# Performance work log

Measured on AMD Instinct MI355X. Metric: run time of the kernel, lower is better.

The kernel has to match this reference:

```python
import jax, jax.numpy as jnp
import numpy as np

N_NODES = 100000


def setup_inputs() -> dict:
    key = jax.random.key(0)
    ks = jax.random.split(key, 7)
    input_dim, hidden_dim = 64, 64
    x = jax.random.normal(ks[0], (N_NODES, input_dim), dtype=jnp.float32)
    edge_index = jax.random.randint(ks[1], (2, 1600000), 0, N_NODES, dtype=jnp.int64)
    weights = jax.random.uniform(ks[2], (N_NODES,), dtype=jnp.float32)
    # MLP params: Linear(input_dim->hidden), ReLU, Linear(hidden->hidden)
    s1 = 1.0 / np.sqrt(input_dim)
    s2 = 1.0 / np.sqrt(hidden_dim)
    W1 = jax.random.uniform(ks[3], (input_dim, hidden_dim), minval=-s1, maxval=s1, dtype=jnp.float32)
    b1 = jax.random.uniform(ks[4], (hidden_dim,), minval=-s1, maxval=s1, dtype=jnp.float32)
    W2 = jax.random.uniform(ks[5], (hidden_dim, hidden_dim), minval=-s2, maxval=s2, dtype=jnp.float32)
    b2 = jax.random.uniform(ks[6], (hidden_dim,), minval=-s2, maxval=s2, dtype=jnp.float32)
    return {"x": x, "edge_index": edge_index, "weights": weights,
            "W1": W1, "b1": b1, "W2": W2, "b2": b2}


def reference(x, edge_index, weights, W1, b1, W2, b2):
    src, dst = edge_index[0], edge_index[1]
    # GINConv (eps=0): h_i = MLP(x_i + sum_{j->i} x_j)
    agg = jax.ops.segment_sum(x[src], dst, num_segments=N_NODES)  # [N, d]
    h = agg + x
    h = jnp.maximum(h @ W1 + b1, 0.0)
    h = h @ W2 + b2                                                # [N, hidden]
    # per-node weighting then sum over nodes -> [1, 1, hidden]
    out = jnp.sum(h * weights[:, None], axis=0)
    return out[None, None, :]
```

## Files before the change

kernel.cpp:

```cpp
#include <hip/hip_runtime.h>
#include <hip/hip_bf16.h>

#define N_NODES 100000
#define N_EDGES 1600000
#define DIM 64
#define NB1 391
#define NGROUPS (N_NODES / 4)
#define NBLK_GM 1792
#define CSTRIDE 100096
#define E4 (N_EDGES / 4)
#define E4BLK 1563

#define OFF_COUNTS8 0
#define OFF_SOUT    800768
#define OFF_TOT     800848
#define OFF_OFFSETS 900944
#define OFF_BSUMS   1000960
#define OFF_CSR     1001472
#define OFF_RANK8   2601472
#define OFF_Y16     3001472

__device__ __forceinline__ float blo(unsigned u) { return __uint_as_float(u << 16); }
__device__ __forceinline__ float bhi(unsigned u) { return __uint_as_float(u & 0xffff0000u); }

__global__ __launch_bounds__(256) void convert_hist_kernel(
    const float* __restrict__ x, unsigned* __restrict__ y,
    const int* __restrict__ dst, int* __restrict__ counts8,
    unsigned* __restrict__ rank8)
{
    int i = blockIdx.x * 256 + threadIdx.x;
    if (i < N_NODES * DIM / 4) {
        float4 v = ((const float4*)x)[i];
        __hip_bfloat162 p0 = __float22bfloat162_rn(make_float2(v.x, v.y));
        __hip_bfloat162 p1 = __float22bfloat162_rn(make_float2(v.z, v.w));
        uint2 o;
        o.x = *reinterpret_cast<unsigned*>(&p0);
        o.y = *reinterpret_cast<unsigned*>(&p1);
        ((uint2*)y)[i] = o;
    }
    if (i < E4) {
        int4 d = ((const int4*)dst)[i];
        int* cnt = counts8 + (blockIdx.x & 7) * CSTRIDE;
        unsigned r0 = (unsigned)atomicAdd(&cnt[d.x], 1);
        unsigned r1 = (unsigned)atomicAdd(&cnt[d.y], 1);
        unsigned r2 = (unsigned)atomicAdd(&cnt[d.z], 1);
        unsigned r3 = (unsigned)atomicAdd(&cnt[d.w], 1);
        rank8[i] = r0 | (r1 << 8) | (r2 << 16) | (r3 << 24);
    }
}

__global__ __launch_bounds__(256) void colsum_blocksum_kernel(
    int* __restrict__ counts8, int* __restrict__ tot, int* __restrict__ bsums)
{
    __shared__ int s[256];
    int t = threadIdx.x;
    int idx = blockIdx.x * 256 + t;
    int run = 0;
    if (idx < N_NODES) {
        #pragma unroll
        for (int k = 0; k < 8; ++k) {
            int v = counts8[k * CSTRIDE + idx];
            counts8[k * CSTRIDE + idx] = run;
            run += v;
        }
        tot[idx] = run;
    }
    s[t] = (idx < N_NODES) ? run : 0;
    __syncthreads();
    for (int d = 128; d > 0; d >>= 1) {
        if (t < d) s[t] += s[t + d];
        __syncthreads();
    }
    if (t == 0) bsums[blockIdx.x] = s[0];
}

__global__ __launch_bounds__(256) void offsets_kernel(
    const int* __restrict__ tot, const int* __restrict__ bsums,
    int* __restrict__ offsets, int* __restrict__ counts8)
{
    __shared__ int s[256];
    __shared__ int base_sh;
    const int t = threadIdx.x;
    const int bid = blockIdx.x;

    int contrib = 0;
    if (t < bid) contrib += bsums[t];
    if (t + 256 < bid) contrib += bsums[t + 256];
    s[t] = contrib;
    __syncthreads();
    for (int d = 128; d > 0; d >>= 1) {
        if (t < d) s[t] += s[t + d];
        __syncthreads();
    }
    if (t == 0) base_sh = s[0];
    __syncthreads();
    const int base = base_sh;
    __syncthreads();

    int idx = bid * 256 + t;
    int c = (idx < N_NODES) ? tot[idx] : 0;
    s[t] = c;
    __syncthreads();
    for (int d = 1; d < 256; d <<= 1) {
        int add = (t >= d) ? s[t - d] : 0;
        __syncthreads();
        s[t] += add;
        __syncthreads();
    }
    int excl = (t == 0) ? 0 : s[t - 1];
    int off = base + excl;
    if (idx < N_NODES) {
        offsets[idx] = off;
        #pragma unroll
        for (int k = 0; k < 8; ++k)
            counts8[k * CSTRIDE + idx] += off;
    }
    if (idx == 0) offsets[N_NODES] = N_EDGES;
}

__global__ __launch_bounds__(256) void fill_kernel(
    const int* __restrict__ src, const int* __restrict__ dst,
    const int* __restrict__ counts8, const unsigned* __restrict__ rank8,
    int* __restrict__ csr)
{
    int e4 = blockIdx.x * 256 + threadIdx.x;
    if (e4 < E4) {
        int4 s = ((const int4*)src)[e4];
        int4 d = ((const int4*)dst)[e4];
        unsigned rp = rank8[e4];
        const int* base = counts8 + (((unsigned)e4 >> 8) & 7) * CSTRIDE;
        csr[base[d.x] + (int)(rp & 255u)]         = s.x;
        csr[base[d.y] + (int)((rp >> 8) & 255u)]  = s.y;
        csr[base[d.z] + (int)((rp >> 16) & 255u)] = s.z;
        csr[base[d.w] + (int)((rp >> 24) & 255u)] = s.w;
    }
}

__global__ __launch_bounds__(256) void gather_mlp_kernel(
    const float* __restrict__ x,
    const unsigned* __restrict__ y16,
    const int* __restrict__ offsets,
    const int* __restrict__ csr,
    const float* __restrict__ weights,
    const float* __restrict__ W1,
    const float* __restrict__ b1,
    float* __restrict__ sout)
{
    __shared__ float W1s[DIM * DIM];
    __shared__ float vbuf[4][4][DIM];
    __shared__ float sred[4][DIM];

    const int tid  = threadIdx.x;
    const int lane = tid & 63;
    const int wave = tid >> 6;
    const int slot = lane >> 3;
    const int h    = lane & 7;

    for (int i = tid; i < DIM * DIM; i += 256) W1s[i] = W1[i];
    __syncthreads();

    const float bias = b1[lane];
    float sacc  = 0.f;
    float swacc = 0.f;

    const uint4* yrows = (const uint4*)y16;
    const int oidx = (lane < 5 ? lane : 4);

    int g = blockIdx.x * 4 + wave;
    int bg[4], dd[4], idxv[4];
    float selfv[4];

    if (g < NGROUPS) {
        int off_l = offsets[g * 4 + oidx];
        #pragma unroll
        for (int n = 0; n < 4; ++n) {
            int b = __builtin_amdgcn_readfirstlane(__shfl(off_l, n));
            int e = __builtin_amdgcn_readfirstlane(__shfl(off_l, n + 1));
            bg[n] = b; dd[n] = e - b;
        }
        #pragma unroll
        for (int n = 0; n < 4; ++n)
            idxv[n] = (lane < dd[n]) ? csr[bg[n] + lane] : 0;
        #pragma unroll
        for (int n = 0; n < 4; ++n)
            selfv[n] = x[(size_t)(g * 4 + n) * DIM + lane];
    }

    while (g < NGROUPS) {
        const int i0 = g * 4;

        uint4 r[4][3];
        #pragma unroll
        for (int n = 0; n < 4; ++n) {
            #pragma unroll
            for (int c = 0; c < 3; ++c) {
                r[n][c] = make_uint4(0u, 0u, 0u, 0u);
                if (c * 8 < dd[n]) {
                    const int e = c * 8 + slot;
                    const int s = __shfl(idxv[n], e);
                    uint4 rr = yrows[(size_t)s * 8 + h];
                    if (e < dd[n]) r[n][c] = rr;
                }
            }
        }

        const int gn = g + NBLK_GM * 4;
        int bgn[4], ddn[4], idxn[4];
        float selfn[4];
        if (gn < NGROUPS) {
            int off_ln = offsets[gn * 4 + oidx];
            #pragma unroll
            for (int n = 0; n < 4; ++n) {
                int b = __builtin_amdgcn_readfirstlane(__shfl(off_ln, n));
                int e = __builtin_amdgcn_readfirstlane(__shfl(off_ln, n + 1));
                bgn[n] = b; ddn[n] = e - b;
            }
            #pragma unroll
            for (int n = 0; n < 4; ++n)
                idxn[n] = (lane < ddn[n]) ? csr[bgn[n] + lane] : 0;
            #pragma unroll
            for (int n = 0; n < 4; ++n)
                selfn[n] = x[(size_t)(gn * 4 + n) * DIM + lane];
        }

        #pragma unroll
        for (int n = 0; n < 4; ++n) {
            float a0 = 0.f, a1 = 0.f, a2 = 0.f, a3 = 0.f;
            float a4 = 0.f, a5 = 0.f, a6 = 0.f, a7 = 0.f;
            #pragma unroll
            for (int c = 0; c < 3; ++c) {
                uint4 rr = r[n][c];
                a0 += blo(rr.x); a1 += bhi(rr.x);
                a2 += blo(rr.y); a3 += bhi(rr.y);
                a4 += blo(rr.z); a5 += bhi(rr.z);
                a6 += blo(rr.w); a7 += bhi(rr.w);
            }
            if (dd[n] > 24) {
                const int dcap = dd[n] <= 64 ? dd[n] : 64;
                for (int c = 3; c * 8 < dcap; ++c) {
                    const int e = c * 8 + slot;
                    const int s = __shfl(idxv[n], e < 64 ? e : 0);
                    if (e < dcap) {
                        uint4 rr = yrows[(size_t)s * 8 + h];
                        a0 += blo(rr.x); a1 += bhi(rr.x);
                        a2 += blo(rr.y); a3 += bhi(rr.y);
                        a4 += blo(rr.z); a5 += bhi(rr.z);
                        a6 += blo(rr.w); a7 += bhi(rr.w);
                    }
                }
                if (dd[n] > 64) {
                    for (int jj = bg[n] + 64; jj < bg[n] + dd[n]; ++jj) {
                        const int s = csr[jj];
                        if (slot == 0) {
                            uint4 rr = yrows[(size_t)s * 8 + h];
                            a0 += blo(rr.x); a1 += bhi(rr.x);
                            a2 += blo(rr.y); a3 += bhi(rr.y);
                            a4 += blo(rr.z); a5 += bhi(rr.z);
                            a6 += blo(rr.w); a7 += bhi(rr.w);
                        }
                    }
                }
            }
            #pragma unroll
            for (int m = 8; m <= 32; m <<= 1) {
                a0 += __shfl_xor(a0, m); a1 += __shfl_xor(a1, m);
                a2 += __shfl_xor(a2, m); a3 += __shfl_xor(a3, m);
                a4 += __shfl_xor(a4, m); a5 += __shfl_xor(a5, m);
                a6 += __shfl_xor(a6, m); a7 += __shfl_xor(a7, m);
            }
            if (lane < 8) {
                *(float4*)&vbuf[wave][n][lane * 8]     = make_float4(a0, a1, a2, a3);
                *(float4*)&vbuf[wave][n][lane * 8 + 4] = make_float4(a4, a5, a6, a7);
            }
            vbuf[wave][n][lane] += selfv[n];
        }

        float a0 = bias, a1 = bias, a2 = bias, a3 = bias;
        #pragma unroll
        for (int k = 0; k < DIM; k += 4) {
            float4 q0 = *(const float4*)&vbuf[wave][0][k];
            float4 q1 = *(const float4*)&vbuf[wave][1][k];
            float4 q2 = *(const float4*)&vbuf[wave][2][k];
            float4 q3 = *(const float4*)&vbuf[wave][3][k];
            float w0 = W1s[(k + 0) * DIM + lane];
            float w1 = W1s[(k + 1) * DIM + lane];
            float w2 = W1s[(k + 2) * DIM + lane];
            float w3 = W1s[(k + 3) * DIM + lane];
            a0 = fmaf(q0.x, w0, a0); a0 = fmaf(q0.y, w1, a0);
            a0 = fmaf(q0.z, w2, a0); a0 = fmaf(q0.w, w3, a0);
            a1 = fmaf(q1.x, w0, a1); a1 = fmaf(q1.y, w1, a1);
            a1 = fmaf(q1.z, w2, a1); a1 = fmaf(q1.w, w3, a1);
            a2 = fmaf(q2.x, w0, a2); a2 = fmaf(q2.y, w1, a2);
            a2 = fmaf(q2.z, w2, a2); a2 = fmaf(q2.w, w3, a2);
            a3 = fmaf(q3.x, w0, a3); a3 = fmaf(q3.y, w1, a3);
            a3 = fmaf(q3.z, w2, a3); a3 = fmaf(q3.w, w3, a3);
        }

        const float wt0 = weights[i0 + 0];
        const float wt1 = weights[i0 + 1];
        const float wt2 = weights[i0 + 2];
        const float wt3 = weights[i0 + 3];
        sacc = fmaf(fmaxf(a0, 0.f), wt0, sacc);
        sacc = fmaf(fmaxf(a1, 0.f), wt1, sacc);
        sacc = fmaf(fmaxf(a2, 0.f), wt2, sacc);
        sacc = fmaf(fmaxf(a3, 0.f), wt3, sacc);
        if (lane == 0) swacc += wt0 + wt1 + wt2 + wt3;

        g = gn;
        #pragma unroll
        for (int n = 0; n < 4; ++n) {
            bg[n] = bgn[n]; dd[n] = ddn[n];
            idxv[n] = idxn[n]; selfv[n] = selfn[n];
        }
    }

    sred[wave][lane] = sacc;
    __syncthreads();
    if (wave == 0) {
        float t = sred[0][lane] + sred[1][lane] + sred[2][lane] + sred[3][lane];
        atomicAdd(&sout[lane], t);
    }
    if (lane == 0) atomicAdd(&sout[DIM], swacc);
}

__global__ void finalize_kernel(
    const float* __restrict__ sout,
    const float* __restrict__ W2,
    const float* __restrict__ b2,
    float* __restrict__ out)
{
    const int j = threadIdx.x;
    const float sw = sout[DIM];
    float acc = sw * b2[j];
    #pragma unroll
    for (int k = 0; k < DIM; ++k)
        acc = fmaf(sout[k], W2[k * DIM + j], acc);
    out[j] = acc;
}

extern "C" void kernel_launch(void* const* d_in, const int* in_sizes, int n_in,
                              void* d_out, int out_size, void* d_ws, size_t ws_size,
                              hipStream_t stream)
{
    const float* x       = (const float*)d_in[0];
    const int*   ei      = (const int*)d_in[1];
    const float* weights = (const float*)d_in[2];
    const float* W1      = (const float*)d_in[3];
    const float* b1      = (const float*)d_in[4];
    const float* W2      = (const float*)d_in[5];
    const float* b2      = (const float*)d_in[6];
    float* out = (float*)d_out;

    const int* src = ei;
    const int* dst = ei + N_EDGES;

    int*      wsI     = (int*)d_ws;
    int*      counts8 = wsI + OFF_COUNTS8;
    float*    soutF   = (float*)(wsI + OFF_SOUT);
    int*      tot     = wsI + OFF_TOT;
    int*      offsets = wsI + OFF_OFFSETS;
    int*      bsums   = wsI + OFF_BSUMS;
    int*      csr     = wsI + OFF_CSR;
    unsigned* rank8   = (unsigned*)(wsI + OFF_RANK8);
    unsigned* y16     = (unsigned*)(wsI + OFF_Y16);

    hipMemsetAsync(d_ws, 0, (size_t)(OFF_SOUT + 80) * sizeof(int), stream);

    convert_hist_kernel   <<<(N_NODES * DIM / 4 + 255) / 256, 256, 0, stream>>>(x, y16, dst, counts8, rank8);
    colsum_blocksum_kernel<<<NB1,    256, 0, stream>>>(counts8, tot, bsums);
    offsets_kernel        <<<NB1,    256, 0, stream>>>(tot, bsums, offsets, counts8);
    fill_kernel           <<<E4BLK,  256, 0, stream>>>(src, dst, counts8, rank8, csr);
    gather_mlp_kernel     <<<NBLK_GM, 256, 0, stream>>>(x, y16, offsets, csr, weights, W1, b1, soutF);
    finalize_kernel       <<<1,       64, 0, stream>>>(soutF, W2, b2, out);
}
```

Measured before the change: 305.6 us.

## Fuse CSR build and gather-MLP into one cooperative persistent kernel

Replaces the memset and six kernel launches with a single cooperative kernel of 1024 blocks that runs each stage in turn, separated by grid-wide barriers. It also removes the software prefetch of the next group's CSR indices in the gather loop and skips unused chunk accumulation. The aim is to cut per-launch overhead and inter-kernel gaps. In exchange, grid.sync costs are added, the gather runs with fewer blocks, and losing the prefetch may expose memory latency. A multi-kernel fallback is kept for when occupancy is too low.

```diff
diff --git a/kernel.cpp b/kernel.cpp
--- a/kernel.cpp
+++ b/kernel.cpp
@@ -1,15 +1,21 @@
 #include <hip/hip_runtime.h>
 #include <hip/hip_bf16.h>
+#include <hip/hip_cooperative_groups.h>
+
+namespace cg = cooperative_groups;
 
 #define N_NODES 100000
 #define N_EDGES 1600000
 #define DIM 64
 #define NB1 391
 #define NGROUPS (N_NODES / 4)
-#define NBLK_GM 1792
+#define NBLK 1024
+#define GSZ (NBLK * 256)
 #define CSTRIDE 100096
 #define E4 (N_EDGES / 4)
 #define E4BLK 1563
+#define ND4 (N_NODES * DIM / 4)
+#define NBLK_GM 1536
 
 #define OFF_COUNTS8 0
 #define OFF_SOUT    800768
@@ -23,134 +29,14 @@
 __device__ __forceinline__ float blo(unsigned u) { return __uint_as_float(u << 16); }
 __device__ __forceinline__ float bhi(unsigned u) { return __uint_as_float(u & 0xffff0000u); }
 
-__global__ __launch_bounds__(256) void convert_hist_kernel(
-    const float* __restrict__ x, unsigned* __restrict__ y,
-    const int* __restrict__ dst, int* __restrict__ counts8,
-    unsigned* __restrict__ rank8)
-{
-    int i = blockIdx.x * 256 + threadIdx.x;
-    if (i < N_NODES * DIM / 4) {
-        float4 v = ((const float4*)x)[i];
-        __hip_bfloat162 p0 = __float22bfloat162_rn(make_float2(v.x, v.y));
-        __hip_bfloat162 p1 = __float22bfloat162_rn(make_float2(v.z, v.w));
-        uint2 o;
-        o.x = *reinterpret_cast<unsigned*>(&p0);
-        o.y = *reinterpret_cast<unsigned*>(&p1);
-        ((uint2*)y)[i] = o;
-    }
-    if (i < E4) {
-        int4 d = ((const int4*)dst)[i];
-        int* cnt = counts8 + (blockIdx.x & 7) * CSTRIDE;
-        unsigned r0 = (unsigned)atomicAdd(&cnt[d.x], 1);
-        unsigned r1 = (unsigned)atomicAdd(&cnt[d.y], 1);
-        unsigned r2 = (unsigned)atomicAdd(&cnt[d.z], 1);
-        unsigned r3 = (unsigned)atomicAdd(&cnt[d.w], 1);
-        rank8[i] = r0 | (r1 << 8) | (r2 << 16) | (r3 << 24);
-    }
-}
-
-__global__ __launch_bounds__(256) void colsum_blocksum_kernel(
-    int* __restrict__ counts8, int* __restrict__ tot, int* __restrict__ bsums)
-{
-    __shared__ int s[256];
-    int t = threadIdx.x;
-    int idx = blockIdx.x * 256 + t;
-    int run = 0;
-    if (idx < N_NODES) {
-        #pragma unroll
-        for (int k = 0; k < 8; ++k) {
-            int v = counts8[k * CSTRIDE + idx];
-            counts8[k * CSTRIDE + idx] = run;
-            run += v;
-        }
-        tot[idx] = run;
-    }
-    s[t] = (idx < N_NODES) ? run : 0;
-    __syncthreads();
-    for (int d = 128; d > 0; d >>= 1) {
-        if (t < d) s[t] += s[t + d];
-        __syncthreads();
-    }
-    if (t == 0) bsums[blockIdx.x] = s[0];
-}
-
-__global__ __launch_bounds__(256) void offsets_kernel(
-    const int* __restrict__ tot, const int* __restrict__ bsums,
-    int* __restrict__ offsets, int* __restrict__ counts8)
-{
-    __shared__ int s[256];
-    __shared__ int base_sh;
-    const int t = threadIdx.x;
-    const int bid = blockIdx.x;
-
-    int contrib = 0;
-    if (t < bid) contrib += bsums[t];
-    if (t + 256 < bid) contrib += bsums[t + 256];
-    s[t] = contrib;
-    __syncthreads();
-    for (int d = 128; d > 0; d >>= 1) {
-        if (t < d) s[t] += s[t + d];
-        __syncthreads();
-    }
-    if (t == 0) base_sh = s[0];
-    __syncthreads();
-    const int base = base_sh;
-    __syncthreads();
-
-    int idx = bid * 256 + t;
-    int c = (idx < N_NODES) ? tot[idx] : 0;
-    s[t] = c;
-    __syncthreads();
-    for (int d = 1; d < 256; d <<= 1) {
-        int add = (t >= d) ? s[t - d] : 0;
-        __syncthreads();
-        s[t] += add;
-        __syncthreads();
-    }
-    int excl = (t == 0) ? 0 : s[t - 1];
-    int off = base + excl;
-    if (idx < N_NODES) {
-        offsets[idx] = off;
-        #pragma unroll
-        for (int k = 0; k < 8; ++k)
-            counts8[k * CSTRIDE + idx] += off;
-    }
-    if (idx == 0) offsets[N_NODES] = N_EDGES;
-}
-
-__global__ __launch_bounds__(256) void fill_kernel(
-    const int* __restrict__ src, const int* __restrict__ dst,
-    const int* __restrict__ counts8, const unsigned* __restrict__ rank8,
-    int* __restrict__ csr)
-{
-    int e4 = blockIdx.x * 256 + threadIdx.x;
-    if (e4 < E4) {
-        int4 s = ((const int4*)src)[e4];
-        int4 d = ((const int4*)dst)[e4];
-        unsigned rp = rank8[e4];
-        const int* base = counts8 + (((unsigned)e4 >> 8) & 7) * CSTRIDE;
-        csr[base[d.x] + (int)(rp & 255u)]         = s.x;
-        csr[base[d.y] + (int)((rp >> 8) & 255u)]  = s.y;
-        csr[base[d.z] + (int)((rp >> 16) & 255u)] = s.z;
-        csr[base[d.w] + (int)((rp >> 24) & 255u)] = s.w;
-    }
-}
-
-__global__ __launch_bounds__(256) void gather_mlp_kernel(
-    const float* __restrict__ x,
-    const unsigned* __restrict__ y16,
-    const int* __restrict__ offsets,
-    const int* __restrict__ csr,
-    const float* __restrict__ weights,
-    const float* __restrict__ W1,
-    const float* __restrict__ b1,
-    float* __restrict__ sout)
-{
-    __shared__ float W1s[DIM * DIM];
-    __shared__ float vbuf[4][4][DIM];
-    __shared__ float sred[4][DIM];
-
-    const int tid  = threadIdx.x;
+__device__ __forceinline__ void gather_mlp_body(
+    const float* __restrict__ x, const unsigned* __restrict__ y16,
+    const int* __restrict__ offsets, const int* __restrict__ csr,
+    const float* __restrict__ weights, const float* __restrict__ W1,
+    const float* __restrict__ b1, float* __restrict__ sout,
+    float (*W1s), float (*vbuf)[4][DIM], float (*sred)[DIM],
+    int gridBlocks, int bid, int tid)
+{
     const int lane = tid & 63;
     const int wave = tid >> 6;
     const int slot = lane >> 3;
@@ -164,30 +50,27 @@
     float swacc = 0.f;
 
     const uint4* yrows = (const uint4*)y16;
-    const int oidx = (lane < 5 ? lane : 4);
-
-    int g = blockIdx.x * 4 + wave;
-    int bg[4], dd[4], idxv[4];
-    float selfv[4];
-
-    if (g < NGROUPS) {
-        int off_l = offsets[g * 4 + oidx];
+
+    for (int g = bid * 4 + wave; g < NGROUPS; g += gridBlocks * 4) {
+        const int i0 = g * 4;
+
+        int off_l = offsets[i0 + (lane < 5 ? lane : 4)];
+        int bg[4], dd[4];
         #pragma unroll
         for (int n = 0; n < 4; ++n) {
             int b = __builtin_amdgcn_readfirstlane(__shfl(off_l, n));
             int e = __builtin_amdgcn_readfirstlane(__shfl(off_l, n + 1));
             bg[n] = b; dd[n] = e - b;
         }
+
+        int idxv[4];
+        float selfv[4];
         #pragma unroll
         for (int n = 0; n < 4; ++n)
             idxv[n] = (lane < dd[n]) ? csr[bg[n] + lane] : 0;
         #pragma unroll
         for (int n = 0; n < 4; ++n)
-            selfv[n] = x[(size_t)(g * 4 + n) * DIM + lane];
-    }
-
-    while (g < NGROUPS) {
-        const int i0 = g * 4;
+            selfv[n] = x[(size_t)(i0 + n) * DIM + lane];
 
         uint4 r[4][3];
         #pragma unroll
@@ -204,36 +87,19 @@
             }
         }
 
-        const int gn = g + NBLK_GM * 4;
-        int bgn[4], ddn[4], idxn[4];
-        float selfn[4];
-        if (gn < NGROUPS) {
-            int off_ln = offsets[gn * 4 + oidx];
-            #pragma unroll
-            for (int n = 0; n < 4; ++n) {
-                int b = __builtin_amdgcn_readfirstlane(__shfl(off_ln, n));
-                int e = __builtin_amdgcn_readfirstlane(__shfl(off_ln, n + 1));
-                bgn[n] = b; ddn[n] = e - b;
-            }
-            #pragma unroll
-            for (int n = 0; n < 4; ++n)
-                idxn[n] = (lane < ddn[n]) ? csr[bgn[n] + lane] : 0;
-            #pragma unroll
-            for (int n = 0; n < 4; ++n)
-                selfn[n] = x[(size_t)(gn * 4 + n) * DIM + lane];
-        }
-
         #pragma unroll
         for (int n = 0; n < 4; ++n) {
             float a0 = 0.f, a1 = 0.f, a2 = 0.f, a3 = 0.f;
             float a4 = 0.f, a5 = 0.f, a6 = 0.f, a7 = 0.f;
             #pragma unroll
             for (int c = 0; c < 3; ++c) {
-                uint4 rr = r[n][c];
-                a0 += blo(rr.x); a1 += bhi(rr.x);
-                a2 += blo(rr.y); a3 += bhi(rr.y);
-                a4 += blo(rr.z); a5 += bhi(rr.z);
-                a6 += blo(rr.w); a7 += bhi(rr.w);
+                if (c * 8 < dd[n]) {
+                    uint4 rr = r[n][c];
+                    a0 += blo(rr.x); a1 += bhi(rr.x);
+                    a2 += blo(rr.y); a3 += bhi(rr.y);
+                    a4 += blo(rr.z); a5 += bhi(rr.z);
+                    a6 += blo(rr.w); a7 += bhi(rr.w);
+                }
             }
             if (dd[n] > 24) {
                 const int dcap = dd[n] <= 64 ? dd[n] : 64;
@@ -305,13 +171,6 @@
         sacc = fmaf(fmaxf(a2, 0.f), wt2, sacc);
         sacc = fmaf(fmaxf(a3, 0.f), wt3, sacc);
         if (lane == 0) swacc += wt0 + wt1 + wt2 + wt3;
-
-        g = gn;
-        #pragma unroll
-        for (int n = 0; n < 4; ++n) {
-            bg[n] = bgn[n]; dd[n] = ddn[n];
-            idxv[n] = idxn[n]; selfv[n] = selfn[n];
-        }
     }
 
     sred[wave][lane] = sacc;
@@ -321,6 +180,274 @@
         atomicAdd(&sout[lane], t);
     }
     if (lane == 0) atomicAdd(&sout[DIM], swacc);
+}
+
+__global__ __launch_bounds__(256, 4) void mega_kernel(
+    const float* __restrict__ x,
+    const int* __restrict__ src,
+    const int* __restrict__ dst,
+    const float* __restrict__ weights,
+    const float* __restrict__ W1,
+    const float* __restrict__ b1,
+    const float* __restrict__ W2,
+    const float* __restrict__ b2,
+    int* __restrict__ ws,
+    float* __restrict__ out)
+{
+    cg::grid_group grid = cg::this_grid();
+
+    __shared__ float W1s[DIM * DIM];
+    __shared__ float vbuf[4][4][DIM];
+    __shared__ float sred[4][DIM];
+    __shared__ int   sscan[256];
+    __shared__ int   base_sh;
+
+    int*      counts8 = ws + OFF_COUNTS8;
+    float*    sout    = (float*)(ws + OFF_SOUT);
+    int*      tot     = ws + OFF_TOT;
+    int*      offsets = ws + OFF_OFFSETS;
+    int*      bsums   = ws + OFF_BSUMS;
+    int*      csr     = ws + OFF_CSR;
+    unsigned* rank8   = (unsigned*)(ws + OFF_RANK8);
+    unsigned* y16     = (unsigned*)(ws + OFF_Y16);
+
+    const int tid  = threadIdx.x;
+    const int bid  = blockIdx.x;
+    const int gtid = bid * 256 + tid;
+
+    for (int i = gtid; i < OFF_SOUT + 80; i += GSZ) ws[i] = 0;
+    grid.sync();
+
+    for (int i = gtid; i < ND4; i += GSZ) {
+        float4 v = ((const float4*)x)[i];
+        __hip_bfloat162 p0 = __float22bfloat162_rn(make_float2(v.x, v.y));
+        __hip_bfloat162 p1 = __float22bfloat162_rn(make_float2(v.z, v.w));
+        uint2 o;
+        o.x = *reinterpret_cast<unsigned*>(&p0);
+        o.y = *reinterpret_cast<unsigned*>(&p1);
+        ((uint2*)y16)[i] = o;
+    }
+    for (int i = gtid; i < E4; i += GSZ) {
+        int4 d = ((const int4*)dst)[i];
+        int* cnt = counts8 + (((unsigned)i >> 8) & 7) * CSTRIDE;
+        unsigned r0 = (unsigned)atomicAdd(&cnt[d.x], 1);
+        unsigned r1 = (unsigned)atomicAdd(&cnt[d.y], 1);
+        unsigned r2 = (unsigned)atomicAdd(&cnt[d.z], 1);
+        unsigned r3 = (unsigned)atomicAdd(&cnt[d.w], 1);
+        rank8[i] = r0 | (r1 << 8) | (r2 << 16) | (r3 << 24);
+    }
+    grid.sync();
+
+    if (bid < NB1) {
+        int idx = bid * 256 + tid;
+        int run = 0;
+        if (idx < N_NODES) {
+            #pragma unroll
+            for (int k = 0; k < 8; ++k) {
+                int v = counts8[k * CSTRIDE + idx];
+                counts8[k * CSTRIDE + idx] = run;
+                run += v;
+            }
+            tot[idx] = run;
+        }
+        sscan[tid] = (idx < N_NODES) ? run : 0;
+        __syncthreads();
+        for (int d = 128; d > 0; d >>= 1) {
+            if (tid < d) sscan[tid] += sscan[tid + d];
+            __syncthreads();
+        }
+        if (tid == 0) bsums[bid] = sscan[0];
+    }
+    grid.sync();
+
+    if (bid < NB1) {
+        int contrib = 0;
+        if (tid < bid) contrib += bsums[tid];
+        if (tid + 256 < bid) contrib += bsums[tid + 256];
+        sscan[tid] = contrib;
+        __syncthreads();
+        for (int d = 128; d > 0; d >>= 1) {
+            if (tid < d) sscan[tid] += sscan[tid + d];
+            __syncthreads();
+        }
+        if (tid == 0) base_sh = sscan[0];
+        __syncthreads();
+        const int base = base_sh;
+        __syncthreads();
+
+        int idx = bid * 256 + tid;
+        int c = (idx < N_NODES) ? tot[idx] : 0;
+        sscan[tid] = c;
+        __syncthreads();
+        for (int d = 1; d < 256; d <<= 1) {
+            int add = (tid >= d) ? sscan[tid - d] : 0;
+            __syncthreads();
+            sscan[tid] += add;
+            __syncthreads();
+        }
+        int excl = (tid == 0) ? 0 : sscan[tid - 1];
+        int off = base + excl;
+        if (idx < N_NODES) {
+            offsets[idx] = off;
+            #pragma unroll
+            for (int k = 0; k < 8; ++k)
+                counts8[k * CSTRIDE + idx] += off;
+        }
+        if (idx == 0) offsets[N_NODES] = N_EDGES;
+    }
+    grid.sync();
+
+    for (int e4 = gtid; e4 < E4; e4 += GSZ) {
+        int4 s = ((const int4*)src)[e4];
+        int4 d = ((const int4*)dst)[e4];
+        unsigned rp = rank8[e4];
+        const int* base = counts8 + (((unsigned)e4 >> 8) & 7) * CSTRIDE;
+        csr[base[d.x] + (int)(rp & 255u)]         = s.x;
+        csr[base[d.y] + (int)((rp >> 8) & 255u)]  = s.y;
+        csr[base[d.z] + (int)((rp >> 16) & 255u)] = s.z;
+        csr[base[d.w] + (int)((rp >> 24) & 255u)] = s.w;
+    }
+    grid.sync();
+
+    gather_mlp_body(x, y16, offsets, csr, weights, W1, b1, sout,
+                    W1s, vbuf, sred, NBLK, bid, tid);
+    grid.sync();
+
+    if (bid == 0 && tid < DIM) {
+        const int j = tid;
+        const float sw = sout[DIM];
+        float acc = sw * b2[j];
+        #pragma unroll
+        for (int k = 0; k < DIM; ++k)
+            acc = fmaf(sout[k], W2[k * DIM + j], acc);
+        out[j] = acc;
+    }
+}
+
+__global__ __launch_bounds__(256) void convert_hist_kernel(
+    const float* __restrict__ x, unsigned* __restrict__ y,
+    const int* __restrict__ dst, int* __restrict__ counts8,
+    unsigned* __restrict__ rank8)
+{
+    int i = blockIdx.x * 256 + threadIdx.x;
+    if (i < ND4) {
+        float4 v = ((const float4*)x)[i];
+        __hip_bfloat162 p0 = __float22bfloat162_rn(make_float2(v.x, v.y));
+        __hip_bfloat162 p1 = __float22bfloat162_rn(make_float2(v.z, v.w));
+        uint2 o;
+        o.x = *reinterpret_cast<unsigned*>(&p0);
+        o.y = *reinterpret_cast<unsigned*>(&p1);
+        ((uint2*)y)[i] = o;
+    }
+    if (i < E4) {
+        int4 d = ((const int4*)dst)[i];
+        int* cnt = counts8 + (((unsigned)i >> 8) & 7) * CSTRIDE;
+        unsigned r0 = (unsigned)atomicAdd(&cnt[d.x], 1);
+        unsigned r1 = (unsigned)atomicAdd(&cnt[d.y], 1);
+        unsigned r2 = (unsigned)atomicAdd(&cnt[d.z], 1);
+        unsigned r3 = (unsigned)atomicAdd(&cnt[d.w], 1);
+        rank8[i] = r0 | (r1 << 8) | (r2 << 16) | (r3 << 24);
+    }
+}
+
+__global__ __launch_bounds__(256) void colsum_blocksum_kernel(
+    int* __restrict__ counts8, int* __restrict__ tot, int* __restrict__ bsums)
+{
+    __shared__ int s[256];
+    int t = threadIdx.x;
+    int idx = blockIdx.x * 256 + t;
+    int run = 0;
+    if (idx < N_NODES) {
+        #pragma unroll
+        for (int k = 0; k < 8; ++k) {
+            int v = counts8[k * CSTRIDE + idx];
+            counts8[k * CSTRIDE + idx] = run;
+            run += v;
+        }
+        tot[idx] = run;
+    }
+    s[t] = (idx < N_NODES) ? run : 0;
+    __syncthreads();
+    for (int d = 128; d > 0; d >>= 1) {
+        if (t < d) s[t] += s[t + d];
+        __syncthreads();
+    }
+    if (t == 0) bsums[blockIdx.x] = s[0];
+}
+
+__global__ __launch_bounds__(256) void offsets_kernel(
+    const int* __restrict__ tot, const int* __restrict__ bsums,
+    int* __restrict__ offsets, int* __restrict__ counts8)
+{
+    __shared__ int s[256];
+    __shared__ int base_sh;
+    const int t = threadIdx.x;
+    const int bid = blockIdx.x;
+
+    int contrib = 0;
+    if (t < bid) contrib += bsums[t];
+    if (t + 256 < bid) contrib += bsums[t + 256];
+    s[t] = contrib;
+    __syncthreads();
+    for (int d = 128; d > 0; d >>= 1) {
+        if (t < d) s[t] += s[t + d];
+        __syncthreads();
+    }
+    if (t == 0) base_sh = s[0];
+    __syncthreads();
+    const int base = base_sh;
+    __syncthreads();
+
+    int idx = bid * 256 + t;
+    int c = (idx < N_NODES) ? tot[idx] : 0;
+    s[t] = c;
+    __syncthreads();
+    for (int d = 1; d < 256; d <<= 1) {
+        int add = (t >= d) ? s[t - d] : 0;
+        __syncthreads();
+        s[t] += add;
+        __syncthreads();
+    }
+    int excl = (t == 0) ? 0 : s[t - 1];
+    int off = base + excl;
+    if (idx < N_NODES) {
+        offsets[idx] = off;
+        #pragma unroll
+        for (int k = 0; k < 8; ++k)
+            counts8[k * CSTRIDE + idx] += off;
+    }
+    if (idx == 0) offsets[N_NODES] = N_EDGES;
+}
+
+__global__ __launch_bounds__(256) void fill_kernel(
+    const int* __restrict__ src, const int* __restrict__ dst,
+    const int* __restrict__ counts8, const unsigned* __restrict__ rank8,
+    int* __restrict__ csr)
+{
+    int e4 = blockIdx.x * 256 + threadIdx.x;
+    if (e4 < E4) {
+        int4 s = ((const int4*)src)[e4];
+        int4 d = ((const int4*)dst)[e4];
+        unsigned rp = rank8[e4];
+        const int* base = counts8 + (((unsigned)e4 >> 8) & 7) * CSTRIDE;
+        csr[base[d.x] + (int)(rp & 255u)]         = s.x;
+        csr[base[d.y] + (int)((rp >> 8) & 255u)]  = s.y;
+        csr[base[d.z] + (int)((rp >> 16) & 255u)] = s.z;
+        csr[base[d.w] + (int)((rp >> 24) & 255u)] = s.w;
+    }
+}
+
+__global__ __launch_bounds__(256) void gather_mlp_kernel(
+    const float* __restrict__ x, const unsigned* __restrict__ y16,
+    const int* __restrict__ offsets, const int* __restrict__ csr,
+    const float* __restrict__ weights, const float* __restrict__ W1,
+    const float* __restrict__ b1, float* __restrict__ sout)
+{
+    __shared__ float W1s[DIM * DIM];
+    __shared__ float vbuf[4][4][DIM];
+    __shared__ float sred[4][DIM];
+    gather_mlp_body(x, y16, offsets, csr, weights, W1, b1, sout,
+                    W1s, vbuf, sred, NBLK_GM, blockIdx.x, threadIdx.x);
 }
 
 __global__ void finalize_kernel(
@@ -353,23 +480,37 @@
 
     const int* src = ei;
     const int* dst = ei + N_EDGES;
-
-    int*      wsI     = (int*)d_ws;
-    int*      counts8 = wsI + OFF_COUNTS8;
-    float*    soutF   = (float*)(wsI + OFF_SOUT);
-    int*      tot     = wsI + OFF_TOT;
-    int*      offsets = wsI + OFF_OFFSETS;
-    int*      bsums   = wsI + OFF_BSUMS;
-    int*      csr     = wsI + OFF_CSR;
-    unsigned* rank8   = (unsigned*)(wsI + OFF_RANK8);
-    unsigned* y16     = (unsigned*)(wsI + OFF_Y16);
-
-    hipMemsetAsync(d_ws, 0, (size_t)(OFF_SOUT + 80) * sizeof(int), stream);
-
-    convert_hist_kernel   <<<(N_NODES * DIM / 4 + 255) / 256, 256, 0, stream>>>(x, y16, dst, counts8, rank8);
-    colsum_blocksum_kernel<<<NB1,    256, 0, stream>>>(counts8, tot, bsums);
-    offsets_kernel        <<<NB1,    256, 0, stream>>>(tot, bsums, offsets, counts8);
-    fill_kernel           <<<E4BLK,  256, 0, stream>>>(src, dst, counts8, rank8, csr);
-    gather_mlp_kernel     <<<NBLK_GM, 256, 0, stream>>>(x, y16, offsets, csr, weights, W1, b1, soutF);
-    finalize_kernel       <<<1,       64, 0, stream>>>(soutF, W2, b2, out);
-}
+    int* wsI = (int*)d_ws;
+
+    int maxb = 0;
+    hipError_t oe = hipOccupancyMaxActiveBlocksPerMultiprocessor(
+        &maxb, (const void*)mega_kernel, 256, 0);
+    bool coop_ok = (oe == hipSuccess) && (maxb >= 4);
+
+    if (coop_ok) {
+        void* args[] = {
+            (void*)&x, (void*)&src, (void*)&dst, (void*)&weights,
+            (void*)&W1, (void*)&b1, (void*)&W2, (void*)&b2,
+            (void*)&wsI, (void*)&out
+        };
+        hipLaunchCooperativeKernel((const void*)mega_kernel,
+                                   dim3(NBLK), dim3(256), args, 0, stream);
+    } else {
+        int*      counts8 = wsI + OFF_COUNTS8;
+        float*    soutF   = (float*)(wsI + OFF_SOUT);
+        int*      tot     = wsI + OFF_TOT;
+        int*      offsets = wsI + OFF_OFFSETS;
+        int*      bsums   = wsI + OFF_BSUMS;
+        int*      csr     = wsI + OFF_CSR;
+        unsigned* rank8   = (unsigned*)(wsI + OFF_RANK8);
+        unsigned* y16     = (unsigned*)(wsI + OFF_Y16);
+
+        hipMemsetAsync(d_ws, 0, (size_t)(OFF_SOUT + 80) * sizeof(int), stream);
+        convert_hist_kernel   <<<(ND4 + 255) / 256, 256, 0, stream>>>(x, y16, dst, counts8, rank8);
+        colsum_blocksum_kernel<<<NB1,    256, 0, stream>>>(counts8, tot, bsums);
+        offsets_kernel        <<<NB1,    256, 0, stream>>>(tot, bsums, offsets, counts8);
+        fill_kernel           <<<E4BLK,  256, 0, stream>>>(src, dst, counts8, rank8, csr);
+        gather_mlp_kernel     <<<NBLK_GM, 256, 0, stream>>>(x, y16, offsets, csr, weights, W1, b1, soutF);
+        finalize_kernel       <<<1,       64, 0, stream>>>(soutF, W2, b2, out);
+    }
+}
```

After: 293.2 us. 1.04x faster.
